# Performance work log

Measured on AMD Instinct MI355X. Metric: run time of the kernel, lower is better.

Reference implementation:

```python
import jax, jax.numpy as jnp
import numpy as np

CONF_THRESHOLD = 0.7

def setup_inputs() -> dict:
    key = jax.random.key(0)
    ks = jax.random.split(key, 8)
    B, T, D, H, GH = 16384, 48, 32, 1024, 128
    s = lambda fan: 1.0 / np.sqrt(fan)
    return {
        "x":   jax.random.normal(ks[0], (B, T, D), jnp.float32),
        "gW1": jax.random.normal(ks[1], (D, GH), jnp.float32) * s(D),
        "gb1": jnp.zeros((GH,), jnp.float32),
        "gW2": jax.random.normal(ks[2], (GH, 2), jnp.float32) * s(GH),
        "gb2": jnp.zeros((2,), jnp.float32),
        "nW1": jax.random.normal(ks[3], (T * D, H), jnp.float32) * s(T * D),
        "nb1": jnp.zeros((H,), jnp.float32),
        "nW2": jax.random.normal(ks[4], (H, 2), jnp.float32) * s(H),
        "nb2": jnp.zeros((2,), jnp.float32),
        "aW1": jax.random.normal(ks[5], (T * D, H), jnp.float32) * s(T * D),
        "ab1": jnp.zeros((H,), jnp.float32),
        "aW2": jax.random.normal(ks[6], (H, 2), jnp.float32) * s(H),
        "ab2": jnp.zeros((2,), jnp.float32),
    }

def _gate(x, gW1, gb1, gW2, gb2):
    # mean-pool over time, 2-layer MLP, softmax -> [B, 2] class probs
    h = jax.nn.relu(jnp.mean(x, axis=1) @ gW1 + gb1)
    return jax.nn.softmax(h @ gW2 + gb2, axis=-1)

def _expert(x_flat, W1, b1, W2, b2):
    return jax.nn.relu(x_flat @ W1 + b1) @ W2 + b2

def reference(x, gW1, gb1, gW2, gb2, nW1, nb1, nW2, nb2, aW1, ab1, aW2, ab2):
    B = x.shape[0]
    gate_outputs = _gate(x, gW1, gb1, gW2, gb2)          # [B, 2]
    gate_probs = jnp.max(gate_outputs, axis=1)           # [B]
    gate_decisions = jnp.argmax(gate_outputs, axis=1)    # [B] in {0,1}

    # adaptive routing: low-confidence samples fall back to the normal expert
    high_conf = gate_probs >= CONF_THRESHOLD
    abnormal_mask = high_conf & (gate_decisions == 1)
    # normal_mask = (high_conf & dec==0) | ~high_conf  == ~abnormal_mask (partition)

    x_flat = x.reshape(B, -1)
    normal_out = _expert(x_flat, nW1, nb1, nW2, nb2)     # [B, 2]
    abnormal_out = _expert(x_flat, aW1, ab1, aW2, ab2)   # [B, 2]
    outputs = jnp.where(abnormal_mask[:, None], abnormal_out, normal_out)
    return outputs, gate_decisions, gate_probs
```

## Files before the change

kernel.cpp:

```cpp
#include <hip/hip_runtime.h>

#define TDIM 48
#define DDIM 32
#define KDIM 1536
#define HDIM 1024
#define GHID 128

typedef unsigned short u16;
typedef __bf16 bf16x8 __attribute__((ext_vector_type(8)));
typedef float  f32x4  __attribute__((ext_vector_type(4)));

typedef const void __attribute__((address_space(1))) gvoid;
typedef void       __attribute__((address_space(3))) lvoid;

__device__ __forceinline__ void gld_lds16(const void* g, void* l) {
    __builtin_amdgcn_global_load_lds((gvoid*)g, (lvoid*)l, 16, 0, 0);
}

__device__ __forceinline__ u16 f2bf(float f) {
    union { float f; unsigned u; } v; v.f = f;
    return (u16)((v.u + 0x7fffu + ((v.u >> 16) & 1u)) >> 16);
}

__global__ __launch_bounds__(256) void gate_kernel(
    const float* __restrict__ x,
    const float* __restrict__ gW1, const float* __restrict__ gb1,
    const float* __restrict__ gW2, const float* __restrict__ gb2,
    u16* __restrict__ Xbf, int* __restrict__ route, int* __restrict__ cnt,
    float* __restrict__ out, float* __restrict__ outDec, float* __restrict__ outProb)
{
    const int wave = threadIdx.x >> 6;
    const int lane = threadIdx.x & 63;
    const int b    = blockIdx.x * 4 + wave;
    if (blockIdx.x == 0 && threadIdx.x < 2) cnt[threadIdx.x] = 0;

    const float* xr = x + (size_t)b * KDIM;
    u16* xo = Xbf + (size_t)b * KDIM;

    double a0 = 0, a1 = 0, a2 = 0, a3 = 0;
#pragma unroll
    for (int i = 0; i < 6; ++i) {
        const int idx = i * 256 + lane * 4;
        f32x4 v = __builtin_nontemporal_load((const f32x4*)(xr + idx));
        ushort4 o;
        o.x = f2bf(v[0]); o.y = f2bf(v[1]); o.z = f2bf(v[2]); o.w = f2bf(v[3]);
        *(ushort4*)(xo + idx) = o;
        a0 += v[0]; a1 += v[1]; a2 += v[2]; a3 += v[3];
    }
#pragma unroll
    for (int m = 8; m <= 32; m <<= 1) {
        a0 += __shfl_xor(a0, m); a1 += __shfl_xor(a1, m);
        a2 += __shfl_xor(a2, m); a3 += __shfl_xor(a3, m);
    }
    __shared__ double xm[4][DDIM];
    if (lane < 8) {
        xm[wave][4 * lane + 0] = a0 / 48.0; xm[wave][4 * lane + 1] = a1 / 48.0;
        xm[wave][4 * lane + 2] = a2 / 48.0; xm[wave][4 * lane + 3] = a3 / 48.0;
    }
    __builtin_amdgcn_wave_barrier();
    __builtin_amdgcn_s_waitcnt(0);
    __threadfence_block();

    double h0 = (double)gb1[lane], h1 = (double)gb1[lane + 64];
#pragma unroll
    for (int d = 0; d < DDIM; ++d) {
        const double xv = xm[wave][d];
        h0 += xv * (double)gW1[d * GHID + lane];
        h1 += xv * (double)gW1[d * GHID + 64 + lane];
    }
    h0 = h0 > 0.0 ? h0 : 0.0;
    h1 = h1 > 0.0 ? h1 : 0.0;
    double z0 = h0 * (double)gW2[lane * 2 + 0] + h1 * (double)gW2[(lane + 64) * 2 + 0];
    double z1 = h0 * (double)gW2[lane * 2 + 1] + h1 * (double)gW2[(lane + 64) * 2 + 1];
#pragma unroll
    for (int m = 1; m <= 32; m <<= 1) {
        z0 += __shfl_xor(z0, m);
        z1 += __shfl_xor(z1, m);
    }
    if (lane == 0) {
        z0 += (double)gb2[0]; z1 += (double)gb2[1];
        const int dec = (z1 > z0) ? 1 : 0;
        const double mz = z0 > z1 ? z0 : z1;
        const double e0 = exp(z0 - mz), e1 = exp(z1 - mz);
        const double p = (e0 > e1 ? e0 : e1) / (e0 + e1);
        const float pf = (float)p;
        outDec[b]  = (float)dec;
        outProb[b] = pf;
        out[2 * b + 0] = 0.f;
        out[2 * b + 1] = 0.f;
        const int high = ((double)pf >= 0.7) ? 1 : 0;
        route[b] = (high && dec) ? 1 : 0;
    }
}

__global__ __launch_bounds__(256) void compact_transpose(
    const int* __restrict__ route, int* __restrict__ perm, int* __restrict__ cnt,
    int Bn,
    const float* __restrict__ nW1, const float* __restrict__ aW1,
    u16* __restrict__ W1t)
{
    __shared__ float tile[32][33];
    const int blk = (int)blockIdx.x;
    const int tid = threadIdx.x;

    if (blk < 64) {
        const int b    = blk * 256 + tid;
        const int lane = tid & 63;
        const int active = (b < Bn);
        const int e = active ? route[b] : 0;
        const unsigned long long m1 = __ballot(active && e == 1);
        const unsigned long long m0 = __ballot(active && e == 0);
        const unsigned long long below = (lane == 63) ? ~0ull >> 1 : ((1ull << lane) - 1);
        int base0 = 0, base1 = 0;
        if (lane == 0) {
            if (m0) base0 = atomicAdd(&cnt[0], (int)__popcll(m0));
            if (m1) base1 = atomicAdd(&cnt[1], (int)__popcll(m1));
        }
        base0 = __shfl(base0, 0);
        base1 = __shfl(base1, 0);
        if (active) {
            const int pos = e ? base1 + (int)__popcll(m1 & below)
                              : base0 + (int)__popcll(m0 & below);
            perm[e * Bn + pos] = b;
        }
    } else {
        int t = blk - 64;
        const int e = t >= (32 * 48);
        t -= e ? (32 * 48) : 0;
        const int bx = t & 31;
        const int by = t >> 5;
        const float* W = e ? aW1 : nW1;
        u16* Wt = W1t + (size_t)e * HDIM * KDIM;
        const int tx = tid & 31;
        const int ty = tid >> 5;
#pragma unroll
        for (int r = 0; r < 32; r += 8)
            tile[ty + r][tx] = W[(size_t)(by * 32 + ty + r) * HDIM + bx * 32 + tx];
        __syncthreads();
#pragma unroll
        for (int r = 0; r < 32; r += 8)
            Wt[(size_t)(bx * 32 + ty + r) * KDIM + by * 32 + tx] = f2bf(tile[tx][ty + r]);
    }
}

__global__ __launch_bounds__(256, 4) void expert_gemm(
    const u16* __restrict__ Xbf, const u16* __restrict__ W1t,
    const float* __restrict__ nb1, const float* __restrict__ nW2,
    const float* __restrict__ nb2,
    const float* __restrict__ ab1, const float* __restrict__ aW2,
    const float* __restrict__ ab2,
    const int* __restrict__ perm, const int* __restrict__ cnt,
    float* __restrict__ out, int Bn, int mBlocks)
{
    __shared__ __align__(16) u16 Alds[128 * 64];
    __shared__ __align__(16) u16 Blds[128 * 64];
    __shared__ int   permLds[128];
    __shared__ float w2Lds[128 * 2];
    __shared__ float b1Lds[128];

    const int tid = threadIdx.x;
    const int f    = (int)blockIdx.x;
    const int g4   = f >> 6;
    const int nIdx = (f >> 3) & 7;
    const int mGlb = g4 * 8 + (f & 7);
    const int e  = mGlb >= mBlocks;
    const int mb = mGlb - (e ? mBlocks : 0);
    const int cntE = cnt[e];
    const int start = mb * 128;
    if (start >= cntE) return;
    const int valid = min(128, cntE - start);

    const int n0 = nIdx * 128;
    const u16*  W1e = W1t + (size_t)e * HDIM * KDIM;
    const float* b1 = e ? ab1 : nb1;
    const float* w2 = e ? aW2 : nW2;
    const float* b2 = e ? ab2 : nb2;

    if (tid < 128) permLds[tid] = perm[e * Bn + min(start + tid, cntE - 1)];
    if (tid >= 128) {
        const int j = tid - 128;
        b1Lds[j]        = b1[n0 + j];
        w2Lds[j * 2 + 0] = w2[(n0 + j) * 2 + 0];
        w2Lds[j * 2 + 1] = w2[(n0 + j) * 2 + 1];
    }
    __syncthreads();

    const int rbase = tid >> 3;
    const int cg    = (tid & 7) ^ (rbase & 7);
    const u16* gA[4]; const u16* gB[4];
#pragma unroll
    for (int j = 0; j < 4; ++j) {
        gA[j] = Xbf + (size_t)permLds[rbase + 32 * j] * KDIM + cg * 8;
        gB[j] = W1e + (size_t)(n0 + rbase + 32 * j) * KDIM + cg * 8;
    }
    u16* la = (u16*)Alds + tid * 8;
    u16* lb = (u16*)Blds + tid * 8;

    const int wave = tid >> 6;
    const int lane = tid & 63;
    const int wm   = (wave & 1) * 64;
    const int wn   = (wave >> 1) * 64;
    const int l15  = lane & 15;
    const int quad = lane >> 4;

    f32x4 acc[4][4];
#pragma unroll
    for (int i = 0; i < 4; ++i)
#pragma unroll
        for (int j = 0; j < 4; ++j) acc[i][j] = (f32x4)0.f;

    for (int k0 = 0; k0 < KDIM; k0 += 64) {
#pragma unroll
        for (int j = 0; j < 4; ++j)
            gld_lds16(gA[j] + k0, la + j * 2048);
#pragma unroll
        for (int j = 0; j < 4; ++j)
            gld_lds16(gB[j] + k0, lb + j * 2048);
        __syncthreads();

#pragma unroll
        for (int t = 0; t < 2; ++t) {
            bf16x8 af[4], bfv[4];
#pragma unroll
            for (int mi = 0; mi < 4; ++mi) {
                const int r = wm + mi * 16 + l15;
                const int p = (t * 4 + quad) ^ (r & 7);
                af[mi] = *reinterpret_cast<const bf16x8*>(&Alds[r * 64 + p * 8]);
            }
#pragma unroll
            for (int ni = 0; ni < 4; ++ni) {
                const int r = wn + ni * 16 + l15;
                const int p = (t * 4 + quad) ^ (r & 7);
                bfv[ni] = *reinterpret_cast<const bf16x8*>(&Blds[r * 64 + p * 8]);
            }
#pragma unroll
            for (int mi = 0; mi < 4; ++mi)
#pragma unroll
                for (int ni = 0; ni < 4; ++ni)
                    acc[mi][ni] = __builtin_amdgcn_mfma_f32_16x16x32_bf16(af[mi], bfv[ni], acc[mi][ni], 0, 0, 0);
        }
        __syncthreads();
    }

    const float b2_0 = (n0 == 0) ? b2[0] : 0.f;
    const float b2_1 = (n0 == 0) ? b2[1] : 0.f;
#pragma unroll
    for (int mi = 0; mi < 4; ++mi) {
        float p0[4] = {0.f, 0.f, 0.f, 0.f};
        float p1[4] = {0.f, 0.f, 0.f, 0.f};
#pragma unroll
        for (int ni = 0; ni < 4; ++ni) {
            const int col = wn + ni * 16 + l15;
            const float w20 = w2Lds[col * 2 + 0];
            const float w21 = w2Lds[col * 2 + 1];
            const float bb  = b1Lds[col];
#pragma unroll
            for (int r = 0; r < 4; ++r) {
                float h = acc[mi][ni][r] + bb;
                h = fmaxf(h, 0.f);
                p0[r] += h * w20;
                p1[r] += h * w21;
            }
        }
#pragma unroll
        for (int m = 1; m <= 8; m <<= 1) {
#pragma unroll
            for (int r = 0; r < 4; ++r) {
                p0[r] += __shfl_xor(p0[r], m);
                p1[r] += __shfl_xor(p1[r], m);
            }
        }
        if (l15 < 4) {
            const int r = l15;
            const int lrow = wm + mi * 16 + quad * 4 + r;
            if (lrow < valid) {
                const int srow = permLds[lrow];
                atomicAdd(&out[srow * 2 + 0], p0[r] + b2_0);
                atomicAdd(&out[srow * 2 + 1], p1[r] + b2_1);
            }
        }
    }
}

extern "C" void kernel_launch(void* const* d_in, const int* in_sizes, int n_in,
                              void* d_out, int out_size, void* d_ws, size_t ws_size,
                              hipStream_t stream) {
    const float* x   = (const float*)d_in[0];
    const float* gW1 = (const float*)d_in[1];
    const float* gb1 = (const float*)d_in[2];
    const float* gW2 = (const float*)d_in[3];
    const float* gb2 = (const float*)d_in[4];
    const float* nW1 = (const float*)d_in[5];
    const float* nb1 = (const float*)d_in[6];
    const float* nW2 = (const float*)d_in[7];
    const float* nb2 = (const float*)d_in[8];
    const float* aW1 = (const float*)d_in[9];
    const float* ab1 = (const float*)d_in[10];
    const float* aW2 = (const float*)d_in[11];
    const float* ab2 = (const float*)d_in[12];

    float* out = (float*)d_out;
    const int Bn = in_sizes[0] / KDIM;

    char* ws = (char*)d_ws;
    size_t off = 0;
    u16* Xbf = (u16*)(ws + off); off += (size_t)Bn * KDIM * sizeof(u16);
    u16* W1t = (u16*)(ws + off); off += (size_t)2 * HDIM * KDIM * sizeof(u16);
    int* perm = (int*)(ws + off); off += (size_t)2 * Bn * sizeof(int);
    int* cnt  = (int*)(ws + off); off += 2 * sizeof(int);
    int* route = (int*)(ws + off); off += (size_t)Bn * sizeof(int);

    gate_kernel<<<Bn / 4, 256, 0, stream>>>(x, gW1, gb1, gW2, gb2,
                                            Xbf, route, cnt,
                                            out, out + 2 * Bn, out + 3 * Bn);

    compact_transpose<<<64 + 2 * (HDIM / 32) * (KDIM / 32), 256, 0, stream>>>(
        route, perm, cnt, Bn, nW1, aW1, W1t);

    const int mBlocks = (Bn + 127) / 128;
    expert_gemm<<<8 * 2 * mBlocks, 256, 0, stream>>>(
        Xbf, W1t, nb1, nW2, nb2, ab1, aW2, ab2, perm, cnt, out, Bn, mBlocks);
}
```

Baseline: 237.0 us.

## Pipeline expert GEMM with 4-stage LDS ring and 256x128 tiles; merge gate+transpose

Replaces the single-buffered 128x128 expert GEMM (with two barriers per 64-wide K step) with a 512-thread, 256x128-tile kernel. It uses a 4-deep ring of 32-wide K slices in LDS, prefetches three slices ahead with direct global-to-LDS loads, and issues MFMAs at raised priority. The weight transpose now runs in the same launch as the gate kernel, and compaction moves to its own small kernel. This is meant to hide global-load latency and overlap the transpose with gating, at the cost of more LDS, lower occupancy, and hand-tuned waitcnt counts that must stay correct.

```diff
diff --git a/kernel.cpp b/kernel.cpp
--- a/kernel.cpp
+++ b/kernel.cpp
@@ -5,6 +5,7 @@
 #define KDIM 1536
 #define HDIM 1024
 #define GHID 128
+#define KTN  48
 
 typedef unsigned short u16;
 typedef __bf16 bf16x8 __attribute__((ext_vector_type(8)));
@@ -22,115 +23,89 @@
     return (u16)((v.u + 0x7fffu + ((v.u >> 16) & 1u)) >> 16);
 }
 
-__global__ __launch_bounds__(256) void gate_kernel(
+__global__ __launch_bounds__(256) void gate_transpose(
     const float* __restrict__ x,
     const float* __restrict__ gW1, const float* __restrict__ gb1,
     const float* __restrict__ gW2, const float* __restrict__ gb2,
     u16* __restrict__ Xbf, int* __restrict__ route, int* __restrict__ cnt,
-    float* __restrict__ out, float* __restrict__ outDec, float* __restrict__ outProb)
+    float* __restrict__ out, float* __restrict__ outDec, float* __restrict__ outProb,
+    const float* __restrict__ nW1, const float* __restrict__ aW1,
+    u16* __restrict__ W1t, int gateBlocks)
 {
-    const int wave = threadIdx.x >> 6;
-    const int lane = threadIdx.x & 63;
-    const int b    = blockIdx.x * 4 + wave;
-    if (blockIdx.x == 0 && threadIdx.x < 2) cnt[threadIdx.x] = 0;
-
-    const float* xr = x + (size_t)b * KDIM;
-    u16* xo = Xbf + (size_t)b * KDIM;
-
-    double a0 = 0, a1 = 0, a2 = 0, a3 = 0;
-#pragma unroll
-    for (int i = 0; i < 6; ++i) {
-        const int idx = i * 256 + lane * 4;
-        f32x4 v = __builtin_nontemporal_load((const f32x4*)(xr + idx));
-        ushort4 o;
-        o.x = f2bf(v[0]); o.y = f2bf(v[1]); o.z = f2bf(v[2]); o.w = f2bf(v[3]);
-        *(ushort4*)(xo + idx) = o;
-        a0 += v[0]; a1 += v[1]; a2 += v[2]; a3 += v[3];
-    }
-#pragma unroll
-    for (int m = 8; m <= 32; m <<= 1) {
-        a0 += __shfl_xor(a0, m); a1 += __shfl_xor(a1, m);
-        a2 += __shfl_xor(a2, m); a3 += __shfl_xor(a3, m);
-    }
     __shared__ double xm[4][DDIM];
-    if (lane < 8) {
-        xm[wave][4 * lane + 0] = a0 / 48.0; xm[wave][4 * lane + 1] = a1 / 48.0;
-        xm[wave][4 * lane + 2] = a2 / 48.0; xm[wave][4 * lane + 3] = a3 / 48.0;
-    }
-    __builtin_amdgcn_wave_barrier();
-    __builtin_amdgcn_s_waitcnt(0);
-    __threadfence_block();
-
-    double h0 = (double)gb1[lane], h1 = (double)gb1[lane + 64];
-#pragma unroll
-    for (int d = 0; d < DDIM; ++d) {
-        const double xv = xm[wave][d];
-        h0 += xv * (double)gW1[d * GHID + lane];
-        h1 += xv * (double)gW1[d * GHID + 64 + lane];
-    }
-    h0 = h0 > 0.0 ? h0 : 0.0;
-    h1 = h1 > 0.0 ? h1 : 0.0;
-    double z0 = h0 * (double)gW2[lane * 2 + 0] + h1 * (double)gW2[(lane + 64) * 2 + 0];
-    double z1 = h0 * (double)gW2[lane * 2 + 1] + h1 * (double)gW2[(lane + 64) * 2 + 1];
-#pragma unroll
-    for (int m = 1; m <= 32; m <<= 1) {
-        z0 += __shfl_xor(z0, m);
-        z1 += __shfl_xor(z1, m);
-    }
-    if (lane == 0) {
-        z0 += (double)gb2[0]; z1 += (double)gb2[1];
-        const int dec = (z1 > z0) ? 1 : 0;
-        const double mz = z0 > z1 ? z0 : z1;
-        const double e0 = exp(z0 - mz), e1 = exp(z1 - mz);
-        const double p = (e0 > e1 ? e0 : e1) / (e0 + e1);
-        const float pf = (float)p;
-        outDec[b]  = (float)dec;
-        outProb[b] = pf;
-        out[2 * b + 0] = 0.f;
-        out[2 * b + 1] = 0.f;
-        const int high = ((double)pf >= 0.7) ? 1 : 0;
-        route[b] = (high && dec) ? 1 : 0;
-    }
-}
-
-__global__ __launch_bounds__(256) void compact_transpose(
-    const int* __restrict__ route, int* __restrict__ perm, int* __restrict__ cnt,
-    int Bn,
-    const float* __restrict__ nW1, const float* __restrict__ aW1,
-    u16* __restrict__ W1t)
-{
     __shared__ float tile[32][33];
-    const int blk = (int)blockIdx.x;
-    const int tid = threadIdx.x;
-
-    if (blk < 64) {
-        const int b    = blk * 256 + tid;
-        const int lane = tid & 63;
-        const int active = (b < Bn);
-        const int e = active ? route[b] : 0;
-        const unsigned long long m1 = __ballot(active && e == 1);
-        const unsigned long long m0 = __ballot(active && e == 0);
-        const unsigned long long below = (lane == 63) ? ~0ull >> 1 : ((1ull << lane) - 1);
-        int base0 = 0, base1 = 0;
+
+    if ((int)blockIdx.x < gateBlocks) {
+        const int wave = threadIdx.x >> 6;
+        const int lane = threadIdx.x & 63;
+        const int b    = blockIdx.x * 4 + wave;
+        if (blockIdx.x == 0 && threadIdx.x < 2) cnt[threadIdx.x] = 0;
+
+        const float* xr = x + (size_t)b * KDIM;
+        u16* xo = Xbf + (size_t)b * KDIM;
+
+        double a0 = 0, a1 = 0, a2 = 0, a3 = 0;
+#pragma unroll
+        for (int i = 0; i < 6; ++i) {
+            const int idx = i * 256 + lane * 4;
+            f32x4 v = __builtin_nontemporal_load((const f32x4*)(xr + idx));
+            ushort4 o;
+            o.x = f2bf(v[0]); o.y = f2bf(v[1]); o.z = f2bf(v[2]); o.w = f2bf(v[3]);
+            *(ushort4*)(xo + idx) = o;
+            a0 += v[0]; a1 += v[1]; a2 += v[2]; a3 += v[3];
+        }
+#pragma unroll
+        for (int m = 8; m <= 32; m <<= 1) {
+            a0 += __shfl_xor(a0, m); a1 += __shfl_xor(a1, m);
+            a2 += __shfl_xor(a2, m); a3 += __shfl_xor(a3, m);
+        }
+        if (lane < 8) {
+            xm[wave][4 * lane + 0] = a0 / 48.0; xm[wave][4 * lane + 1] = a1 / 48.0;
+            xm[wave][4 * lane + 2] = a2 / 48.0; xm[wave][4 * lane + 3] = a3 / 48.0;
+        }
+        __builtin_amdgcn_wave_barrier();
+        __builtin_amdgcn_s_waitcnt(0);
+        __threadfence_block();
+
+        double h0 = (double)gb1[lane], h1 = (double)gb1[lane + 64];
+#pragma unroll
+        for (int d = 0; d < DDIM; ++d) {
+            const double xv = xm[wave][d];
+            h0 += xv * (double)gW1[d * GHID + lane];
+            h1 += xv * (double)gW1[d * GHID + 64 + lane];
+        }
+        h0 = h0 > 0.0 ? h0 : 0.0;
+        h1 = h1 > 0.0 ? h1 : 0.0;
+        double z0 = h0 * (double)gW2[lane * 2 + 0] + h1 * (double)gW2[(lane + 64) * 2 + 0];
+        double z1 = h0 * (double)gW2[lane * 2 + 1] + h1 * (double)gW2[(lane + 64) * 2 + 1];
+#pragma unroll
+        for (int m = 1; m <= 32; m <<= 1) {
+            z0 += __shfl_xor(z0, m);
+            z1 += __shfl_xor(z1, m);
+        }
         if (lane == 0) {
-            if (m0) base0 = atomicAdd(&cnt[0], (int)__popcll(m0));
-            if (m1) base1 = atomicAdd(&cnt[1], (int)__popcll(m1));
-        }
-        base0 = __shfl(base0, 0);
-        base1 = __shfl(base1, 0);
-        if (active) {
-            const int pos = e ? base1 + (int)__popcll(m1 & below)
-                              : base0 + (int)__popcll(m0 & below);
-            perm[e * Bn + pos] = b;
+            z0 += (double)gb2[0]; z1 += (double)gb2[1];
+            const int dec = (z1 > z0) ? 1 : 0;
+            const double mz = z0 > z1 ? z0 : z1;
+            const double e0 = exp(z0 - mz), e1 = exp(z1 - mz);
+            const double p = (e0 > e1 ? e0 : e1) / (e0 + e1);
+            const float pf = (float)p;
+            outDec[b]  = (float)dec;
+            outProb[b] = pf;
+            out[2 * b + 0] = 0.f;
+            out[2 * b + 1] = 0.f;
+            const int high = ((double)pf >= 0.7) ? 1 : 0;
+            route[b] = (high && dec) ? 1 : 0;
         }
     } else {
-        int t = blk - 64;
+        int t = (int)blockIdx.x - gateBlocks;
         const int e = t >= (32 * 48);
         t -= e ? (32 * 48) : 0;
         const int bx = t & 31;
         const int by = t >> 5;
         const float* W = e ? aW1 : nW1;
         u16* Wt = W1t + (size_t)e * HDIM * KDIM;
+        const int tid = threadIdx.x;
         const int tx = tid & 31;
         const int ty = tid >> 5;
 #pragma unroll
@@ -143,63 +118,96 @@
     }
 }
 
-__global__ __launch_bounds__(256, 4) void expert_gemm(
+__global__ __launch_bounds__(256) void compact_kernel(
+    const int* __restrict__ route, int* __restrict__ perm, int* __restrict__ cnt,
+    int Bn)
+{
+    const int tid  = threadIdx.x;
+    const int b    = (int)blockIdx.x * 256 + tid;
+    const int lane = tid & 63;
+    const int active = (b < Bn);
+    const int e = active ? route[b] : 0;
+    const unsigned long long m1 = __ballot(active && e == 1);
+    const unsigned long long m0 = __ballot(active && e == 0);
+    const unsigned long long below = (lane == 63) ? ~0ull >> 1 : ((1ull << lane) - 1);
+    int base0 = 0, base1 = 0;
+    if (lane == 0) {
+        if (m0) base0 = atomicAdd(&cnt[0], (int)__popcll(m0));
+        if (m1) base1 = atomicAdd(&cnt[1], (int)__popcll(m1));
+    }
+    base0 = __shfl(base0, 0);
+    base1 = __shfl(base1, 0);
+    if (active) {
+        const int pos = e ? base1 + (int)__popcll(m1 & below)
+                          : base0 + (int)__popcll(m0 & below);
+        perm[e * Bn + pos] = b;
+    }
+}
+
+__global__ __launch_bounds__(512, 2) void expert_gemm(
     const u16* __restrict__ Xbf, const u16* __restrict__ W1t,
     const float* __restrict__ nb1, const float* __restrict__ nW2,
     const float* __restrict__ nb2,
     const float* __restrict__ ab1, const float* __restrict__ aW2,
     const float* __restrict__ ab2,
     const int* __restrict__ perm, const int* __restrict__ cnt,
-    float* __restrict__ out, int Bn, int mBlocks)
+    float* __restrict__ out, int Bn, int mB)
 {
-    __shared__ __align__(16) u16 Alds[128 * 64];
-    __shared__ __align__(16) u16 Blds[128 * 64];
-    __shared__ int   permLds[128];
+    __shared__ __align__(16) u16 Ab[4][256 * 32];
+    __shared__ __align__(16) u16 Bb[4][128 * 32];
+    __shared__ int   permLds[256];
     __shared__ float w2Lds[128 * 2];
     __shared__ float b1Lds[128];
 
     const int tid = threadIdx.x;
-    const int f    = (int)blockIdx.x;
-    const int g4   = f >> 6;
-    const int nIdx = (f >> 3) & 7;
-    const int mGlb = g4 * 8 + (f & 7);
-    const int e  = mGlb >= mBlocks;
-    const int mb = mGlb - (e ? mBlocks : 0);
+    const int L    = (int)blockIdx.x;
+    const int m    = (L & 7) + 8 * (L >> 6);
+    const int nIdx = (L >> 3) & 7;
+    const int e  = m >= mB;
+    const int mb = m - (e ? mB : 0);
     const int cntE = cnt[e];
-    const int start = mb * 128;
+    const int start = mb * 256;
     if (start >= cntE) return;
-    const int valid = min(128, cntE - start);
-
+    const int valid = min(256, cntE - start);
     const int n0 = nIdx * 128;
+
     const u16*  W1e = W1t + (size_t)e * HDIM * KDIM;
     const float* b1 = e ? ab1 : nb1;
     const float* w2 = e ? aW2 : nW2;
     const float* b2 = e ? ab2 : nb2;
 
-    if (tid < 128) permLds[tid] = perm[e * Bn + min(start + tid, cntE - 1)];
-    if (tid >= 128) {
-        const int j = tid - 128;
-        b1Lds[j]        = b1[n0 + j];
+    if (tid < 256) {
+        permLds[tid] = perm[e * Bn + min(start + tid, cntE - 1)];
+    } else if (tid < 384) {
+        const int j = tid - 256;
+        b1Lds[j]         = b1[n0 + j];
         w2Lds[j * 2 + 0] = w2[(n0 + j) * 2 + 0];
         w2Lds[j * 2 + 1] = w2[(n0 + j) * 2 + 1];
     }
     __syncthreads();
 
-    const int rbase = tid >> 3;
-    const int cg    = (tid & 7) ^ (rbase & 7);
-    const u16* gA[4]; const u16* gB[4];
-#pragma unroll
-    for (int j = 0; j < 4; ++j) {
-        gA[j] = Xbf + (size_t)permLds[rbase + 32 * j] * KDIM + cg * 8;
-        gB[j] = W1e + (size_t)(n0 + rbase + 32 * j) * KDIM + cg * 8;
-    }
-    u16* la = (u16*)Alds + tid * 8;
-    u16* lb = (u16*)Blds + tid * 8;
+    const int rQ = tid >> 2;
+    const int cg = (tid & 3) ^ ((tid >> 3) & 3);
+    const u16* gA0 = Xbf + (size_t)permLds[rQ]       * KDIM + cg * 8;
+    const u16* gA1 = Xbf + (size_t)permLds[rQ + 128] * KDIM + cg * 8;
+    const u16* gB  = W1e + (size_t)(n0 + rQ)         * KDIM + cg * 8;
+    const int dA0 = tid * 8;
+    const int dA1 = tid * 8 + 4096;
+    const int dB  = tid * 8;
+
+#pragma unroll
+    for (int pk = 0; pk < 3; ++pk) {
+        gld_lds16(gA0 + pk * 32, &Ab[pk][dA0]);
+        gld_lds16(gA1 + pk * 32, &Ab[pk][dA1]);
+        gld_lds16(gB  + pk * 32, &Bb[pk][dB]);
+    }
+    asm volatile("s_waitcnt vmcnt(6)" ::: "memory");
+    asm volatile("s_barrier" ::: "memory");
 
     const int wave = tid >> 6;
     const int lane = tid & 63;
-    const int wm   = (wave & 1) * 64;
-    const int wn   = (wave >> 1) * 64;
+    const int wm   = (wave >> 1) * 64;
+    const int wn   = (wave & 1) * 64;
     const int l15  = lane & 15;
     const int quad = lane >> 4;
 
@@ -209,37 +217,45 @@
 #pragma unroll
         for (int j = 0; j < 4; ++j) acc[i][j] = (f32x4)0.f;
 
-    for (int k0 = 0; k0 < KDIM; k0 += 64) {
-#pragma unroll
-        for (int j = 0; j < 4; ++j)
-            gld_lds16(gA[j] + k0, la + j * 2048);
-#pragma unroll
-        for (int j = 0; j < 4; ++j)
-            gld_lds16(gB[j] + k0, lb + j * 2048);
-        __syncthreads();
-
-#pragma unroll
-        for (int t = 0; t < 2; ++t) {
-            bf16x8 af[4], bfv[4];
-#pragma unroll
-            for (int mi = 0; mi < 4; ++mi) {
-                const int r = wm + mi * 16 + l15;
-                const int p = (t * 4 + quad) ^ (r & 7);
-                af[mi] = *reinterpret_cast<const bf16x8*>(&Alds[r * 64 + p * 8]);
-            }
-#pragma unroll
-            for (int ni = 0; ni < 4; ++ni) {
-                const int r = wn + ni * 16 + l15;
-                const int p = (t * 4 + quad) ^ (r & 7);
-                bfv[ni] = *reinterpret_cast<const bf16x8*>(&Blds[r * 64 + p * 8]);
-            }
-#pragma unroll
-            for (int mi = 0; mi < 4; ++mi)
-#pragma unroll
-                for (int ni = 0; ni < 4; ++ni)
-                    acc[mi][ni] = __builtin_amdgcn_mfma_f32_16x16x32_bf16(af[mi], bfv[ni], acc[mi][ni], 0, 0, 0);
-        }
-        __syncthreads();
+#pragma unroll 4
+    for (int kt = 0; kt < KTN; ++kt) {
+        const int buf = kt & 3;
+        bf16x8 af[4], bfv[4];
+#pragma unroll
+        for (int mi = 0; mi < 4; ++mi) {
+            const int r = wm + mi * 16 + l15;
+            const int p = quad ^ ((r >> 1) & 3);
+            af[mi] = *reinterpret_cast<const bf16x8*>(&Ab[buf][r * 32 + p * 8]);
+        }
+#pragma unroll
+        for (int ni = 0; ni < 4; ++ni) {
+            const int r = wn + ni * 16 + l15;
+            const int p = quad ^ ((r >> 1) & 3);
+            bfv[ni] = *reinterpret_cast<const bf16x8*>(&Bb[buf][r * 32 + p * 8]);
+        }
+        if (kt < KTN - 3) {
+            const int b3 = (kt + 3) & 3;
+            const int k3 = (kt + 3) * 32;
+            gld_lds16(gA0 + k3, &Ab[b3][dA0]);
+            gld_lds16(gA1 + k3, &Ab[b3][dA1]);
+            gld_lds16(gB  + k3, &Bb[b3][dB]);
+        }
+        asm volatile("s_barrier" ::: "memory");
+        asm volatile("s_waitcnt lgkmcnt(0)" ::: "memory");
+        __builtin_amdgcn_sched_barrier(0);
+        __builtin_amdgcn_s_setprio(1);
+#pragma unroll
+        for (int mi = 0; mi < 4; ++mi)
+#pragma unroll
+            for (int ni = 0; ni < 4; ++ni)
+                acc[mi][ni] = __builtin_amdgcn_mfma_f32_16x16x32_bf16(
+                    af[mi], bfv[ni], acc[mi][ni], 0, 0, 0);
+        __builtin_amdgcn_s_setprio(0);
+        __builtin_amdgcn_sched_barrier(0);
+        if (kt < KTN - 3)       { asm volatile("s_waitcnt vmcnt(6)" ::: "memory"); }
+        else if (kt == KTN - 3) { asm volatile("s_waitcnt vmcnt(3)" ::: "memory"); }
+        else                    { asm volatile("s_waitcnt vmcnt(0)" ::: "memory"); }
+        asm volatile("s_barrier" ::: "memory");
     }
 
     const float b2_0 = (n0 == 0) ? b2[0] : 0.f;
@@ -263,11 +279,11 @@
             }
         }
 #pragma unroll
-        for (int m = 1; m <= 8; m <<= 1) {
+        for (int mm = 1; mm <= 8; mm <<= 1) {
 #pragma unroll
             for (int r = 0; r < 4; ++r) {
-                p0[r] += __shfl_xor(p0[r], m);
-                p1[r] += __shfl_xor(p1[r], m);
+                p0[r] += __shfl_xor(p0[r], mm);
+                p1[r] += __shfl_xor(p1[r], mm);
             }
         }
         if (l15 < 4) {
@@ -310,14 +326,16 @@
     int* cnt  = (int*)(ws + off); off += 2 * sizeof(int);
     int* route = (int*)(ws + off); off += (size_t)Bn * sizeof(int);
 
-    gate_kernel<<<Bn / 4, 256, 0, stream>>>(x, gW1, gb1, gW2, gb2,
-                                            Xbf, route, cnt,
-                                            out, out + 2 * Bn, out + 3 * Bn);
-
-    compact_transpose<<<64 + 2 * (HDIM / 32) * (KDIM / 32), 256, 0, stream>>>(
-        route, perm, cnt, Bn, nW1, aW1, W1t);
-
-    const int mBlocks = (Bn + 127) / 128;
-    expert_gemm<<<8 * 2 * mBlocks, 256, 0, stream>>>(
-        Xbf, W1t, nb1, nW2, nb2, ab1, aW2, ab2, perm, cnt, out, Bn, mBlocks);
-}
+    const int gateBlocks = Bn / 4;
+    const int trBlocks   = 2 * (HDIM / 32) * (KDIM / 32);
+
+    gate_transpose<<<gateBlocks + trBlocks, 256, 0, stream>>>(
+        x, gW1, gb1, gW2, gb2, Xbf, route, cnt,
+        out, out + 2 * Bn, out + 3 * Bn, nW1, aW1, W1t, gateBlocks);
+
+    compact_kernel<<<(Bn + 255) / 256, 256, 0, stream>>>(route, perm, cnt, Bn);
+
+    const int mB = (Bn + 255) / 256;
+    expert_gemm<<<2 * mB * (HDIM / 128), 512, 0, stream>>>(
+        Xbf, W1t, nb1, nW2, nb2, ab1, aW2, ab2, perm, cnt, out, Bn, mB);
+}
```

New measurement: 255.4 us. 1.08x slower.

## Fuse gate, routing compaction and weight transpose into one kernel launch

Applied to the files above, without the earlier changes.

Merges the gate kernel and the compact/transpose kernel into one launch. Gate blocks now do per-block compaction: four samples per block, with two atomics per block writing perm directly, so the route buffer and its extra pass go away. The counter reset moves to a hipMemsetAsync. This removes a launch and its serialisation point, and lets the weight transpose overlap with the gate work. In exchange it adds many more global atomics (4096 blocks instead of 64 waves) and a memset node.

```diff
diff --git a/kernel.cpp b/kernel.cpp
--- a/kernel.cpp
+++ b/kernel.cpp
@@ -22,115 +22,105 @@
     return (u16)((v.u + 0x7fffu + ((v.u >> 16) & 1u)) >> 16);
 }
 
-__global__ __launch_bounds__(256) void gate_kernel(
+__global__ __launch_bounds__(256) void gate_transpose(
     const float* __restrict__ x,
     const float* __restrict__ gW1, const float* __restrict__ gb1,
     const float* __restrict__ gW2, const float* __restrict__ gb2,
-    u16* __restrict__ Xbf, int* __restrict__ route, int* __restrict__ cnt,
-    float* __restrict__ out, float* __restrict__ outDec, float* __restrict__ outProb)
+    u16* __restrict__ Xbf, int* __restrict__ perm, int* __restrict__ cnt,
+    float* __restrict__ out, float* __restrict__ outDec, float* __restrict__ outProb,
+    const float* __restrict__ nW1, const float* __restrict__ aW1,
+    u16* __restrict__ W1t, int gateBlocks, int Bn)
 {
-    const int wave = threadIdx.x >> 6;
-    const int lane = threadIdx.x & 63;
-    const int b    = blockIdx.x * 4 + wave;
-    if (blockIdx.x == 0 && threadIdx.x < 2) cnt[threadIdx.x] = 0;
-
-    const float* xr = x + (size_t)b * KDIM;
-    u16* xo = Xbf + (size_t)b * KDIM;
-
-    double a0 = 0, a1 = 0, a2 = 0, a3 = 0;
-#pragma unroll
-    for (int i = 0; i < 6; ++i) {
-        const int idx = i * 256 + lane * 4;
-        f32x4 v = __builtin_nontemporal_load((const f32x4*)(xr + idx));
-        ushort4 o;
-        o.x = f2bf(v[0]); o.y = f2bf(v[1]); o.z = f2bf(v[2]); o.w = f2bf(v[3]);
-        *(ushort4*)(xo + idx) = o;
-        a0 += v[0]; a1 += v[1]; a2 += v[2]; a3 += v[3];
-    }
-#pragma unroll
-    for (int m = 8; m <= 32; m <<= 1) {
-        a0 += __shfl_xor(a0, m); a1 += __shfl_xor(a1, m);
-        a2 += __shfl_xor(a2, m); a3 += __shfl_xor(a3, m);
-    }
     __shared__ double xm[4][DDIM];
-    if (lane < 8) {
-        xm[wave][4 * lane + 0] = a0 / 48.0; xm[wave][4 * lane + 1] = a1 / 48.0;
-        xm[wave][4 * lane + 2] = a2 / 48.0; xm[wave][4 * lane + 3] = a3 / 48.0;
-    }
-    __builtin_amdgcn_wave_barrier();
-    __builtin_amdgcn_s_waitcnt(0);
-    __threadfence_block();
-
-    double h0 = (double)gb1[lane], h1 = (double)gb1[lane + 64];
-#pragma unroll
-    for (int d = 0; d < DDIM; ++d) {
-        const double xv = xm[wave][d];
-        h0 += xv * (double)gW1[d * GHID + lane];
-        h1 += xv * (double)gW1[d * GHID + 64 + lane];
-    }
-    h0 = h0 > 0.0 ? h0 : 0.0;
-    h1 = h1 > 0.0 ? h1 : 0.0;
-    double z0 = h0 * (double)gW2[lane * 2 + 0] + h1 * (double)gW2[(lane + 64) * 2 + 0];
-    double z1 = h0 * (double)gW2[lane * 2 + 1] + h1 * (double)gW2[(lane + 64) * 2 + 1];
-#pragma unroll
-    for (int m = 1; m <= 32; m <<= 1) {
-        z0 += __shfl_xor(z0, m);
-        z1 += __shfl_xor(z1, m);
-    }
-    if (lane == 0) {
-        z0 += (double)gb2[0]; z1 += (double)gb2[1];
-        const int dec = (z1 > z0) ? 1 : 0;
-        const double mz = z0 > z1 ? z0 : z1;
-        const double e0 = exp(z0 - mz), e1 = exp(z1 - mz);
-        const double p = (e0 > e1 ? e0 : e1) / (e0 + e1);
-        const float pf = (float)p;
-        outDec[b]  = (float)dec;
-        outProb[b] = pf;
-        out[2 * b + 0] = 0.f;
-        out[2 * b + 1] = 0.f;
-        const int high = ((double)pf >= 0.7) ? 1 : 0;
-        route[b] = (high && dec) ? 1 : 0;
-    }
-}
-
-__global__ __launch_bounds__(256) void compact_transpose(
-    const int* __restrict__ route, int* __restrict__ perm, int* __restrict__ cnt,
-    int Bn,
-    const float* __restrict__ nW1, const float* __restrict__ aW1,
-    u16* __restrict__ W1t)
-{
     __shared__ float tile[32][33];
-    const int blk = (int)blockIdx.x;
-    const int tid = threadIdx.x;
-
-    if (blk < 64) {
-        const int b    = blk * 256 + tid;
-        const int lane = tid & 63;
-        const int active = (b < Bn);
-        const int e = active ? route[b] : 0;
-        const unsigned long long m1 = __ballot(active && e == 1);
-        const unsigned long long m0 = __ballot(active && e == 0);
-        const unsigned long long below = (lane == 63) ? ~0ull >> 1 : ((1ull << lane) - 1);
-        int base0 = 0, base1 = 0;
+    __shared__ int eSh[4];
+
+    if ((int)blockIdx.x < gateBlocks) {
+        const int wave = threadIdx.x >> 6;
+        const int lane = threadIdx.x & 63;
+        const int b    = blockIdx.x * 4 + wave;
+
+        const float* xr = x + (size_t)b * KDIM;
+        u16* xo = Xbf + (size_t)b * KDIM;
+
+        double a0 = 0, a1 = 0, a2 = 0, a3 = 0;
+#pragma unroll
+        for (int i = 0; i < 6; ++i) {
+            const int idx = i * 256 + lane * 4;
+            f32x4 v = __builtin_nontemporal_load((const f32x4*)(xr + idx));
+            ushort4 o;
+            o.x = f2bf(v[0]); o.y = f2bf(v[1]); o.z = f2bf(v[2]); o.w = f2bf(v[3]);
+            *(ushort4*)(xo + idx) = o;
+            a0 += v[0]; a1 += v[1]; a2 += v[2]; a3 += v[3];
+        }
+#pragma unroll
+        for (int m = 8; m <= 32; m <<= 1) {
+            a0 += __shfl_xor(a0, m); a1 += __shfl_xor(a1, m);
+            a2 += __shfl_xor(a2, m); a3 += __shfl_xor(a3, m);
+        }
+        if (lane < 8) {
+            xm[wave][4 * lane + 0] = a0 / 48.0; xm[wave][4 * lane + 1] = a1 / 48.0;
+            xm[wave][4 * lane + 2] = a2 / 48.0; xm[wave][4 * lane + 3] = a3 / 48.0;
+        }
+        __builtin_amdgcn_wave_barrier();
+        __builtin_amdgcn_s_waitcnt(0);
+        __threadfence_block();
+
+        double h0 = (double)gb1[lane], h1 = (double)gb1[lane + 64];
+#pragma unroll
+        for (int d = 0; d < DDIM; ++d) {
+            const double xv = xm[wave][d];
+            h0 += xv * (double)gW1[d * GHID + lane];
+            h1 += xv * (double)gW1[d * GHID + 64 + lane];
+        }
+        h0 = h0 > 0.0 ? h0 : 0.0;
+        h1 = h1 > 0.0 ? h1 : 0.0;
+        double z0 = h0 * (double)gW2[lane * 2 + 0] + h1 * (double)gW2[(lane + 64) * 2 + 0];
+        double z1 = h0 * (double)gW2[lane * 2 + 1] + h1 * (double)gW2[(lane + 64) * 2 + 1];
+#pragma unroll
+        for (int m = 1; m <= 32; m <<= 1) {
+            z0 += __shfl_xor(z0, m);
+            z1 += __shfl_xor(z1, m);
+        }
         if (lane == 0) {
-            if (m0) base0 = atomicAdd(&cnt[0], (int)__popcll(m0));
-            if (m1) base1 = atomicAdd(&cnt[1], (int)__popcll(m1));
-        }
-        base0 = __shfl(base0, 0);
-        base1 = __shfl(base1, 0);
-        if (active) {
-            const int pos = e ? base1 + (int)__popcll(m1 & below)
-                              : base0 + (int)__popcll(m0 & below);
-            perm[e * Bn + pos] = b;
+            z0 += (double)gb2[0]; z1 += (double)gb2[1];
+            const int dec = (z1 > z0) ? 1 : 0;
+            const double mz = z0 > z1 ? z0 : z1;
+            const double e0 = exp(z0 - mz), e1 = exp(z1 - mz);
+            const double p = (e0 > e1 ? e0 : e1) / (e0 + e1);
+            const float pf = (float)p;
+            outDec[b]  = (float)dec;
+            outProb[b] = pf;
+            out[2 * b + 0] = 0.f;
+            out[2 * b + 1] = 0.f;
+            const int high = ((double)pf >= 0.7) ? 1 : 0;
+            eSh[wave] = (high && dec) ? 1 : 0;
+        }
+        __syncthreads();
+        if (threadIdx.x == 0) {
+            const int e0 = eSh[0], e1 = eSh[1], e2 = eSh[2], e3 = eSh[3];
+            const int c1 = e0 + e1 + e2 + e3;
+            const int c0 = 4 - c1;
+            const int base0 = c0 ? atomicAdd(&cnt[0], c0) : 0;
+            const int base1 = c1 ? atomicAdd(&cnt[1], c1) : 0;
+            const int b0 = blockIdx.x * 4;
+            int r0 = 0, r1 = 0;
+#pragma unroll
+            for (int i = 0; i < 4; ++i) {
+                const int e = eSh[i];
+                const int pos = e ? (base1 + r1++) : (base0 + r0++);
+                perm[e * Bn + pos] = b0 + i;
+            }
         }
     } else {
-        int t = blk - 64;
+        int t = (int)blockIdx.x - gateBlocks;
         const int e = t >= (32 * 48);
         t -= e ? (32 * 48) : 0;
         const int bx = t & 31;
         const int by = t >> 5;
         const float* W = e ? aW1 : nW1;
         u16* Wt = W1t + (size_t)e * HDIM * KDIM;
+        const int tid = threadIdx.x;
         const int tx = tid & 31;
         const int ty = tid >> 5;
 #pragma unroll
@@ -308,14 +298,15 @@
     u16* W1t = (u16*)(ws + off); off += (size_t)2 * HDIM * KDIM * sizeof(u16);
     int* perm = (int*)(ws + off); off += (size_t)2 * Bn * sizeof(int);
     int* cnt  = (int*)(ws + off); off += 2 * sizeof(int);
-    int* route = (int*)(ws + off); off += (size_t)Bn * sizeof(int);
-
-    gate_kernel<<<Bn / 4, 256, 0, stream>>>(x, gW1, gb1, gW2, gb2,
-                                            Xbf, route, cnt,
-                                            out, out + 2 * Bn, out + 3 * Bn);
-
-    compact_transpose<<<64 + 2 * (HDIM / 32) * (KDIM / 32), 256, 0, stream>>>(
-        route, perm, cnt, Bn, nW1, aW1, W1t);
+
+    hipMemsetAsync(cnt, 0, 2 * sizeof(int), stream);
+
+    const int gateBlocks = Bn / 4;
+    const int trBlocks   = 2 * (HDIM / 32) * (KDIM / 32);
+
+    gate_transpose<<<gateBlocks + trBlocks, 256, 0, stream>>>(
+        x, gW1, gb1, gW2, gb2, Xbf, perm, cnt,
+        out, out + 2 * Bn, out + 3 * Bn, nW1, aW1, W1t, gateBlocks, Bn);
 
     const int mBlocks = (Bn + 127) / 128;
     expert_gemm<<<8 * 2 * mBlocks, 256, 0, stream>>>(
```

Measured after the change: 259.2 us. 9.3% more time.
